# Kernel tuning notes

Measured on AMD Instinct MI355X. Metric: run time of the kernel, lower is better.

## Reference

```python
import jax, jax.numpy as jnp
import numpy as np

BETA = 0.5
ITEM_NUM = 100000
REGION_NUM = 1000
EMBED = 128
HIDDEN = 256
B, H = 1024, 256


def setup_inputs() -> dict:
    key = jax.random.key(0)
    ks = jax.random.split(key, 10)
    history = jax.random.randint(ks[0], (B, H), 0, ITEM_NUM)
    target = jax.random.randint(ks[1], (B,), 0, ITEM_NUM)
    history_region = jax.random.randint(ks[2], (B, H), 0, REGION_NUM)
    target_region = jax.random.randint(ks[3], (B,), 0, REGION_NUM)
    E_hist = 0.01 * jax.random.normal(ks[4], (ITEM_NUM, EMBED), dtype=jnp.float32)
    E_targ = 0.01 * jax.random.normal(ks[5], (ITEM_NUM, EMBED), dtype=jnp.float32)
    E_reg = 0.01 * jax.random.normal(ks[6], (REGION_NUM, EMBED), dtype=jnp.float32)
    lim1 = 1.0 / np.sqrt(2 * EMBED)
    W1 = jax.random.uniform(ks[7], (2 * EMBED, HIDDEN), jnp.float32, -lim1, lim1)
    b1 = jnp.zeros((HIDDEN,), jnp.float32)
    lim2 = 1.0 / np.sqrt(HIDDEN)
    w2 = jax.random.uniform(ks[8], (HIDDEN,), jnp.float32, -lim2, lim2)
    return {"history": history, "target": target,
            "history_region": history_region, "target_region": target_region,
            "E_hist": E_hist, "E_targ": E_targ, "E_reg": E_reg,
            "W1": W1, "b1": b1, "w2": w2}


def reference(history, target, history_region, target_region,
              E_hist, E_targ, E_reg, W1, b1, w2):
    # gathers + concat: hist [B,H,2d], tgt [B,2d]
    hist = jnp.concatenate([E_hist[history], E_reg[history_region]], axis=-1)
    tgt = jnp.concatenate([E_targ[target], E_reg[target_region]], axis=-1)
    # elementwise product broadcast over history dim
    inp = hist * tgt[:, None, :]                      # [B,H,2d]
    hid = jax.nn.relu(jnp.einsum('bhd,dk->bhk', inp, W1) + b1)
    scores = jnp.einsum('bhk,k->bh', hid, w2)         # [B,H]
    mask = (history != target[:, None]).astype(scores.dtype)
    exp_a = jnp.exp(scores) * mask                    # [B,H]
    denom = jnp.power(jnp.sum(exp_a, axis=-1), BETA)  # [B]
    attn = exp_a / denom[:, None]                     # [B,H]
    # weighted reduction: sum_h sum_d hist*attn*tgt
    pred = jnp.einsum('bhd,bh,bd->b', hist, attn, tgt)
    return jax.nn.sigmoid(pred)
```

## Files before the change

### kernel.cpp

```cpp
#include <hip/hip_runtime.h>
#include <hip/hip_bf16.h>

#define NB 1024
#define NH 256
#define EMB 128
#define TWOD 256
#define HID 256
#define ROWS 128
#define NBLK (NB * 2)

typedef __attribute__((ext_vector_type(4))) float f32x4;
typedef __attribute__((ext_vector_type(8))) short bf16x8;

__device__ __forceinline__ unsigned short f2bf(float f) {
  union { float f; unsigned u; } v; v.f = f;
  unsigned u = v.u;
  unsigned r = (u + 0x7fffu + ((u >> 16) & 1u)) >> 16;
  return (unsigned short)r;
}

__global__ __launch_bounds__(256) void prep_w1t(const float* __restrict__ W1,
                                                unsigned short* __restrict__ W1T) {
  const int d = blockIdx.x;
  const int n = threadIdx.x;
  W1T[(size_t)n * TWOD + d] = f2bf(W1[(size_t)d * HID + n]);
}

__global__ __launch_bounds__(256) void prep_tgt(const int* __restrict__ target,
                                                const int* __restrict__ tregion,
                                                const float* __restrict__ E_targ,
                                                const float* __restrict__ E_reg,
                                                float* __restrict__ tgtv) {
  const int b = blockIdx.x;
  const int c = threadIdx.x;
  float v = (c < EMB) ? E_targ[(size_t)target[b] * EMB + c]
                      : E_reg[(size_t)tregion[b] * EMB + (c - EMB)];
  tgtv[(size_t)b * TWOD + c] = v;
}

__global__ __launch_bounds__(256) void zero_acc(float* __restrict__ p) {
  p[blockIdx.x * 256 + threadIdx.x] = 0.f;
}

__global__ __launch_bounds__(512, 4) void nais_main(
    const int* __restrict__ history, const int* __restrict__ target,
    const int* __restrict__ hregion,
    const float* __restrict__ E_hist, const float* __restrict__ E_reg,
    const unsigned short* __restrict__ W1T, const float* __restrict__ b1,
    const float* __restrict__ w2, const float* __restrict__ tgtv,
    float* __restrict__ acc_se, float* __restrict__ acc_sd)
{
  const int blk = blockIdx.x;
  const int b = blk >> 1;
  const int r0 = (blk & 1) * ROWS;
  const int tid = threadIdx.x;
  const int lane = tid & 63;
  const int wave = tid >> 6;
  const int l15 = lane & 15;
  const int lhi = lane >> 4;
  const int l31 = lane & 31;
  const int halfsel = lane >> 5;

  __shared__ __align__(16) unsigned short inp_lds[ROWS * 256];
  __shared__ float dot_lds[ROWS];
  __shared__ float score_parts[8][ROWS];

  const int tgt_item = target[b];

  {
    const f32x4 t = *(const f32x4*)(tgtv + (size_t)b * TWOD + halfsel * EMB + l31 * 4);
    const int* keysrc = halfsel ? hregion : history;
    const float* table = halfsel ? E_reg : E_hist;

    int key[16];
    #pragma unroll
    for (int s = 0; s < 16; ++s)
      key[s] = keysrc[b * NH + r0 + wave * 16 + s];

    f32x4 vb[16];
    #pragma unroll
    for (int s = 0; s < 16; ++s)
      vb[s] = *(const f32x4*)(table + (size_t)key[s] * EMB + l31 * 4);

    #pragma unroll
    for (int s = 0; s < 16; ++s) {
      const int row = wave * 16 + s;
      f32x4 v = vb[s] * t;
      float ds = v[0] + v[1] + v[2] + v[3];
      ds += __shfl_xor(ds, 1);
      ds += __shfl_xor(ds, 2);
      ds += __shfl_xor(ds, 4);
      ds += __shfl_xor(ds, 8);
      ds += __shfl_xor(ds, 16);
      ds += __shfl_xor(ds, 32);
      if (lane == 0) dot_lds[row] = ds;

      float2 f01; f01.x = v[0]; f01.y = v[1];
      float2 f23; f23.x = v[2]; f23.y = v[3];
      __hip_bfloat162 p0 = __float22bfloat162_rn(f01);
      __hip_bfloat162 p1 = __float22bfloat162_rn(f23);
      union { __hip_bfloat162 h; unsigned u; } c0, c1;
      c0.h = p0; c1.h = p1;
      const int g = halfsel * 16 + (l31 >> 1);
      const int gs = g ^ (row & 7) ^ ((g >> 3) & 3);
      unsigned* dst = (unsigned*)&inp_lds[row * 256 + gs * 8 + (lane & 1) * 4];
      dst[0] = c0.u; dst[1] = c1.u;
    }
  }
  __syncthreads();

  bf16x8 bfr[8][2];
  float b1v[2], w2v[2];
  #pragma unroll
  for (int n = 0; n < 2; ++n) {
    const int colh = wave * 32 + n * 16 + l15;
    b1v[n] = b1[colh];
    w2v[n] = w2[colh];
    #pragma unroll
    for (int kk = 0; kk < 8; ++kk)
      bfr[kk][n] = *(const bf16x8*)(W1T + (size_t)colh * TWOD + kk * 32 + lhi * 8);
  }

  #pragma unroll
  for (int c = 0; c < 2; ++c) {
    f32x4 acc[4][2];
    #pragma unroll
    for (int m = 0; m < 4; ++m)
      #pragma unroll
      for (int n = 0; n < 2; ++n)
        acc[m][n] = (f32x4){0.f, 0.f, 0.f, 0.f};

    #pragma unroll
    for (int kk = 0; kk < 8; ++kk) {
      bf16x8 af[4];
      #pragma unroll
      for (int m = 0; m < 4; ++m) {
        const int row = c * 64 + m * 16 + l15;
        const int gk = kk * 4 + lhi;
        const int gs = gk ^ (row & 7) ^ ((gk >> 3) & 3);
        af[m] = *(const bf16x8*)(&inp_lds[row * 256 + gs * 8]);
      }
      #pragma unroll
      for (int m = 0; m < 4; ++m)
        #pragma unroll
        for (int n = 0; n < 2; ++n)
          acc[m][n] = __builtin_amdgcn_mfma_f32_16x16x32_bf16(af[m], bfr[kk][n], acc[m][n], 0, 0, 0);
    }

    #pragma unroll
    for (int m = 0; m < 4; ++m) {
      #pragma unroll
      for (int r = 0; r < 4; ++r) {
        float p = 0.f;
        #pragma unroll
        for (int n = 0; n < 2; ++n) {
          float hv = acc[m][n][r] + b1v[n];
          hv = hv > 0.f ? hv : 0.f;
          p += hv * w2v[n];
        }
        p += __shfl_xor(p, 1);
        p += __shfl_xor(p, 2);
        p += __shfl_xor(p, 4);
        p += __shfl_xor(p, 8);
        if (l15 == 0) score_parts[wave][c * 64 + m * 16 + lhi * 4 + r] = p;
      }
    }
  }
  __syncthreads();

  if (wave < 2) {
    const int lrow = wave * 64 + lane;
    float sc = 0.f;
    #pragma unroll
    for (int w = 0; w < 8; ++w) sc += score_parts[w][lrow];
    const int item = history[b * NH + r0 + lrow];
    float e = (item != tgt_item) ? expf(sc) : 0.f;
    float ed = e * dot_lds[lrow];
    #pragma unroll
    for (int off = 32; off >= 1; off >>= 1) {
      e += __shfl_xor(e, off);
      ed += __shfl_xor(ed, off);
    }
    if (lane == 0) {
      atomicAdd(&acc_se[b], e);
      atomicAdd(&acc_sd[b], ed);
    }
  }
}

__global__ __launch_bounds__(256) void finalize(const float* __restrict__ acc_se,
                                                const float* __restrict__ acc_sd,
                                                float* __restrict__ out) {
  const int b = blockIdx.x * 256 + threadIdx.x;
  if (b < NB) {
    const float se = acc_se[b];
    const float sd = acc_sd[b];
    const float pred = (se > 0.f) ? (sd / sqrtf(se)) : 0.f;
    out[b] = 1.f / (1.f + expf(-pred));
  }
}

extern "C" void kernel_launch(void* const* d_in, const int* in_sizes, int n_in,
                              void* d_out, int out_size, void* d_ws, size_t ws_size,
                              hipStream_t stream) {
  const int* history = (const int*)d_in[0];
  const int* target  = (const int*)d_in[1];
  const int* hregion = (const int*)d_in[2];
  const int* tregion = (const int*)d_in[3];
  const float* E_hist = (const float*)d_in[4];
  const float* E_targ = (const float*)d_in[5];
  const float* E_reg  = (const float*)d_in[6];
  const float* W1 = (const float*)d_in[7];
  const float* b1 = (const float*)d_in[8];
  const float* w2 = (const float*)d_in[9];
  float* out = (float*)d_out;

  unsigned short* W1T = (unsigned short*)d_ws;
  char* p = (char*)d_ws + (size_t)TWOD * HID * sizeof(unsigned short);
  float* tgtv = (float*)p;           p += (size_t)NB * TWOD * sizeof(float);
  float* acc_se = (float*)p;         p += (size_t)NB * sizeof(float);
  float* acc_sd = (float*)p;

  zero_acc<<<(2 * NB) / 256, 256, 0, stream>>>(acc_se);
  prep_w1t<<<TWOD, HID, 0, stream>>>(W1, W1T);
  prep_tgt<<<NB, TWOD, 0, stream>>>(target, tregion, E_targ, E_reg, tgtv);
  nais_main<<<NBLK, 512, 0, stream>>>(history, target, hregion, E_hist, E_reg,
                                      W1T, b1, w2, tgtv, acc_se, acc_sd);
  finalize<<<(NB + 255) / 256, 256, 0, stream>>>(acc_se, acc_sd, out);
}
```

Before: 96.34 us.

## Split each batch row across four 256-thread blocks and drop atomics

Each block now handles 64 history rows with 4 waves instead of 128 rows with 8 waves, giving 4096 smaller blocks and halving LDS per block. Each wave now covers 64 hidden columns in two passes, reloading a W1 slice per pass. Per-block partial sums are written to a buffer and summed in finalize, which removes the zeroing kernel and the atomics. MFMA loops are also wrapped in s_setprio. The risk is doubled W1 fragment loads per block and more block-launch overhead.

```diff
diff --git a/kernel.cpp b/kernel.cpp
--- a/kernel.cpp
+++ b/kernel.cpp
@@ -6,8 +6,9 @@
 #define EMB 128
 #define TWOD 256
 #define HID 256
-#define ROWS 128
-#define NBLK (NB * 2)
+#define ROWS 64
+#define BPB 4
+#define NBLK (NB * BPB)
 
 typedef __attribute__((ext_vector_type(4))) float f32x4;
 typedef __attribute__((ext_vector_type(8))) short bf16x8;
@@ -38,21 +39,17 @@
   tgtv[(size_t)b * TWOD + c] = v;
 }
 
-__global__ __launch_bounds__(256) void zero_acc(float* __restrict__ p) {
-  p[blockIdx.x * 256 + threadIdx.x] = 0.f;
-}
-
-__global__ __launch_bounds__(512, 4) void nais_main(
+__global__ __launch_bounds__(256, 4) void nais_main(
     const int* __restrict__ history, const int* __restrict__ target,
     const int* __restrict__ hregion,
     const float* __restrict__ E_hist, const float* __restrict__ E_reg,
     const unsigned short* __restrict__ W1T, const float* __restrict__ b1,
     const float* __restrict__ w2, const float* __restrict__ tgtv,
-    float* __restrict__ acc_se, float* __restrict__ acc_sd)
+    float* __restrict__ part_se, float* __restrict__ part_sd)
 {
   const int blk = blockIdx.x;
-  const int b = blk >> 1;
-  const int r0 = (blk & 1) * ROWS;
+  const int b = blk >> 2;
+  const int r0 = (blk & 3) * ROWS;
   const int tid = threadIdx.x;
   const int lane = tid & 63;
   const int wave = tid >> 6;
@@ -109,20 +106,22 @@
   }
   __syncthreads();
 
-  bf16x8 bfr[8][2];
-  float b1v[2], w2v[2];
   #pragma unroll
-  for (int n = 0; n < 2; ++n) {
-    const int colh = wave * 32 + n * 16 + l15;
-    b1v[n] = b1[colh];
-    w2v[n] = w2[colh];
-    #pragma unroll
-    for (int kk = 0; kk < 8; ++kk)
-      bfr[kk][n] = *(const bf16x8*)(W1T + (size_t)colh * TWOD + kk * 32 + lhi * 8);
-  }
-
-  #pragma unroll
-  for (int c = 0; c < 2; ++c) {
+  for (int cp = 0; cp < 2; ++cp) {
+    const int col0 = wave * 64 + cp * 32;
+
+    bf16x8 bfr[8][2];
+    float b1v[2], w2v[2];
+    #pragma unroll
+    for (int n = 0; n < 2; ++n) {
+      const int colh = col0 + n * 16 + l15;
+      b1v[n] = b1[colh];
+      w2v[n] = w2[colh];
+      #pragma unroll
+      for (int kk = 0; kk < 8; ++kk)
+        bfr[kk][n] = *(const bf16x8*)(W1T + (size_t)colh * TWOD + kk * 32 + lhi * 8);
+    }
+
     f32x4 acc[4][2];
     #pragma unroll
     for (int m = 0; m < 4; ++m)
@@ -130,12 +129,13 @@
       for (int n = 0; n < 2; ++n)
         acc[m][n] = (f32x4){0.f, 0.f, 0.f, 0.f};
 
+    __builtin_amdgcn_s_setprio(1);
     #pragma unroll
     for (int kk = 0; kk < 8; ++kk) {
       bf16x8 af[4];
       #pragma unroll
       for (int m = 0; m < 4; ++m) {
-        const int row = c * 64 + m * 16 + l15;
+        const int row = m * 16 + l15;
         const int gk = kk * 4 + lhi;
         const int gs = gk ^ (row & 7) ^ ((gk >> 3) & 3);
         af[m] = *(const bf16x8*)(&inp_lds[row * 256 + gs * 8]);
@@ -146,7 +146,9 @@
         for (int n = 0; n < 2; ++n)
           acc[m][n] = __builtin_amdgcn_mfma_f32_16x16x32_bf16(af[m], bfr[kk][n], acc[m][n], 0, 0, 0);
     }
-
+    __builtin_amdgcn_s_setprio(0);
+
+    const int strip = wave * 2 + cp;
     #pragma unroll
     for (int m = 0; m < 4; ++m) {
       #pragma unroll
@@ -162,39 +164,42 @@
         p += __shfl_xor(p, 2);
         p += __shfl_xor(p, 4);
         p += __shfl_xor(p, 8);
-        if (l15 == 0) score_parts[wave][c * 64 + m * 16 + lhi * 4 + r] = p;
+        if (l15 == 0) score_parts[strip][m * 16 + lhi * 4 + r] = p;
       }
     }
   }
   __syncthreads();
 
-  if (wave < 2) {
-    const int lrow = wave * 64 + lane;
+  if (wave == 0) {
     float sc = 0.f;
     #pragma unroll
-    for (int w = 0; w < 8; ++w) sc += score_parts[w][lrow];
-    const int item = history[b * NH + r0 + lrow];
+    for (int w = 0; w < 8; ++w) sc += score_parts[w][lane];
+    const int item = history[b * NH + r0 + lane];
     float e = (item != tgt_item) ? expf(sc) : 0.f;
-    float ed = e * dot_lds[lrow];
+    float ed = e * dot_lds[lane];
     #pragma unroll
     for (int off = 32; off >= 1; off >>= 1) {
       e += __shfl_xor(e, off);
       ed += __shfl_xor(ed, off);
     }
     if (lane == 0) {
-      atomicAdd(&acc_se[b], e);
-      atomicAdd(&acc_sd[b], ed);
-    }
-  }
-}
-
-__global__ __launch_bounds__(256) void finalize(const float* __restrict__ acc_se,
-                                                const float* __restrict__ acc_sd,
+      part_se[blk] = e;
+      part_sd[blk] = ed;
+    }
+  }
+}
+
+__global__ __launch_bounds__(256) void finalize(const float* __restrict__ part_se,
+                                                const float* __restrict__ part_sd,
                                                 float* __restrict__ out) {
   const int b = blockIdx.x * 256 + threadIdx.x;
   if (b < NB) {
-    const float se = acc_se[b];
-    const float sd = acc_sd[b];
+    float se = 0.f, sd = 0.f;
+    #pragma unroll
+    for (int i = 0; i < BPB; ++i) {
+      se += part_se[b * BPB + i];
+      sd += part_sd[b * BPB + i];
+    }
     const float pred = (se > 0.f) ? (sd / sqrtf(se)) : 0.f;
     out[b] = 1.f / (1.f + expf(-pred));
   }
@@ -218,13 +223,12 @@
   unsigned short* W1T = (unsigned short*)d_ws;
   char* p = (char*)d_ws + (size_t)TWOD * HID * sizeof(unsigned short);
   float* tgtv = (float*)p;           p += (size_t)NB * TWOD * sizeof(float);
-  float* acc_se = (float*)p;         p += (size_t)NB * sizeof(float);
-  float* acc_sd = (float*)p;
-
-  zero_acc<<<(2 * NB) / 256, 256, 0, stream>>>(acc_se);
+  float* part_se = (float*)p;        p += (size_t)NBLK * sizeof(float);
+  float* part_sd = (float*)p;
+
   prep_w1t<<<TWOD, HID, 0, stream>>>(W1, W1T);
   prep_tgt<<<NB, TWOD, 0, stream>>>(target, tregion, E_targ, E_reg, tgtv);
-  nais_main<<<NBLK, 512, 0, stream>>>(history, target, hregion, E_hist, E_reg,
-                                      W1T, b1, w2, tgtv, acc_se, acc_sd);
-  finalize<<<(NB + 255) / 256, 256, 0, stream>>>(acc_se, acc_sd, out);
-}
+  nais_main<<<NBLK, 256, 0, stream>>>(history, target, hregion, E_hist, E_reg,
+                                      W1T, b1, w2, tgtv, part_se, part_sd);
+  finalize<<<(NB + 255) / 256, 256, 0, stream>>>(part_se, part_sd, out);
+}
```

New measurement: 102.4 us. 6.3% more time.

## Fuse target gather into main kernel and replace atomics with partial sums

Applied to the files above, without the earlier changes.

Removes the prep_tgt and zero_acc launches by gathering the target embedding directly in the main kernel. Per-block results go to a partial-sum buffer instead of atomicAdd, and finalize reduces those partials. History keys are cached in LDS so they are not reloaded from global memory. The MFMA loop now loads W1T fragments per k-step instead of holding them all in registers, and wraps the MFMAs in s_setprio. The aims are fewer launches and lower register pressure, at the cost of more global loads of W1T.

```diff
diff --git a/kernel.cpp b/kernel.cpp
--- a/kernel.cpp
+++ b/kernel.cpp
@@ -7,7 +7,8 @@
 #define TWOD 256
 #define HID 256
 #define ROWS 128
-#define NBLK (NB * 2)
+#define BPB 2
+#define NBLK (NB * BPB)
 
 typedef __attribute__((ext_vector_type(4))) float f32x4;
 typedef __attribute__((ext_vector_type(8))) short bf16x8;
@@ -26,29 +27,14 @@
   W1T[(size_t)n * TWOD + d] = f2bf(W1[(size_t)d * HID + n]);
 }
 
-__global__ __launch_bounds__(256) void prep_tgt(const int* __restrict__ target,
-                                                const int* __restrict__ tregion,
-                                                const float* __restrict__ E_targ,
-                                                const float* __restrict__ E_reg,
-                                                float* __restrict__ tgtv) {
-  const int b = blockIdx.x;
-  const int c = threadIdx.x;
-  float v = (c < EMB) ? E_targ[(size_t)target[b] * EMB + c]
-                      : E_reg[(size_t)tregion[b] * EMB + (c - EMB)];
-  tgtv[(size_t)b * TWOD + c] = v;
-}
-
-__global__ __launch_bounds__(256) void zero_acc(float* __restrict__ p) {
-  p[blockIdx.x * 256 + threadIdx.x] = 0.f;
-}
-
 __global__ __launch_bounds__(512, 4) void nais_main(
     const int* __restrict__ history, const int* __restrict__ target,
-    const int* __restrict__ hregion,
-    const float* __restrict__ E_hist, const float* __restrict__ E_reg,
+    const int* __restrict__ hregion, const int* __restrict__ tregion,
+    const float* __restrict__ E_hist, const float* __restrict__ E_targ,
+    const float* __restrict__ E_reg,
     const unsigned short* __restrict__ W1T, const float* __restrict__ b1,
-    const float* __restrict__ w2, const float* __restrict__ tgtv,
-    float* __restrict__ acc_se, float* __restrict__ acc_sd)
+    const float* __restrict__ w2,
+    float* __restrict__ part_se, float* __restrict__ part_sd)
 {
   const int blk = blockIdx.x;
   const int b = blk >> 1;
@@ -63,15 +49,18 @@
 
   __shared__ __align__(16) unsigned short inp_lds[ROWS * 256];
   __shared__ float dot_lds[ROWS];
+  __shared__ int items_lds[ROWS];
   __shared__ float score_parts[8][ROWS];
 
+  const float* tsrc = halfsel ? (E_reg + (size_t)tregion[b] * EMB)
+                              : (E_targ + (size_t)target[b] * EMB);
+  const f32x4 t = *(const f32x4*)(tsrc + l31 * 4);
   const int tgt_item = target[b];
 
+  const int* keysrc = halfsel ? hregion : history;
+  const float* table = halfsel ? E_reg : E_hist;
+
   {
-    const f32x4 t = *(const f32x4*)(tgtv + (size_t)b * TWOD + halfsel * EMB + l31 * 4);
-    const int* keysrc = halfsel ? hregion : history;
-    const float* table = halfsel ? E_reg : E_hist;
-
     int key[16];
     #pragma unroll
     for (int s = 0; s < 16; ++s)
@@ -85,6 +74,7 @@
     #pragma unroll
     for (int s = 0; s < 16; ++s) {
       const int row = wave * 16 + s;
+      if (lane == 0) items_lds[row] = key[s];
       f32x4 v = vb[s] * t;
       float ds = v[0] + v[1] + v[2] + v[3];
       ds += __shfl_xor(ds, 1);
@@ -109,60 +99,73 @@
   }
   __syncthreads();
 
-  bf16x8 bfr[8][2];
-  float b1v[2], w2v[2];
-  #pragma unroll
-  for (int n = 0; n < 2; ++n) {
-    const int colh = wave * 32 + n * 16 + l15;
-    b1v[n] = b1[colh];
-    w2v[n] = w2[colh];
-    #pragma unroll
-    for (int kk = 0; kk < 8; ++kk)
-      bfr[kk][n] = *(const bf16x8*)(W1T + (size_t)colh * TWOD + kk * 32 + lhi * 8);
-  }
-
-  #pragma unroll
-  for (int c = 0; c < 2; ++c) {
-    f32x4 acc[4][2];
-    #pragma unroll
-    for (int m = 0; m < 4; ++m)
-      #pragma unroll
-      for (int n = 0; n < 2; ++n)
-        acc[m][n] = (f32x4){0.f, 0.f, 0.f, 0.f};
+  {
+    const int col0 = wave * 32;
+    float b1v[2], w2v[2];
+    #pragma unroll
+    for (int n = 0; n < 2; ++n) {
+      const int colh = col0 + n * 16 + l15;
+      b1v[n] = b1[colh];
+      w2v[n] = w2[colh];
+    }
+
+    f32x4 acc[2][4][2];
+    #pragma unroll
+    for (int c = 0; c < 2; ++c)
+      #pragma unroll
+      for (int m = 0; m < 4; ++m)
+        #pragma unroll
+        for (int n = 0; n < 2; ++n)
+          acc[c][m][n] = (f32x4){0.f, 0.f, 0.f, 0.f};
 
     #pragma unroll
     for (int kk = 0; kk < 8; ++kk) {
-      bf16x8 af[4];
+      bf16x8 bfr[2];
+      #pragma unroll
+      for (int n = 0; n < 2; ++n) {
+        const int colh = col0 + n * 16 + l15;
+        bfr[n] = *(const bf16x8*)(W1T + (size_t)colh * TWOD + kk * 32 + lhi * 8);
+      }
+      bf16x8 af[2][4];
+      #pragma unroll
+      for (int c = 0; c < 2; ++c)
+        #pragma unroll
+        for (int m = 0; m < 4; ++m) {
+          const int row = c * 64 + m * 16 + l15;
+          const int gk = kk * 4 + lhi;
+          const int gs = gk ^ (row & 7) ^ ((gk >> 3) & 3);
+          af[c][m] = *(const bf16x8*)(&inp_lds[row * 256 + gs * 8]);
+        }
+      __builtin_amdgcn_s_setprio(1);
+      #pragma unroll
+      for (int c = 0; c < 2; ++c)
+        #pragma unroll
+        for (int m = 0; m < 4; ++m)
+          #pragma unroll
+          for (int n = 0; n < 2; ++n)
+            acc[c][m][n] = __builtin_amdgcn_mfma_f32_16x16x32_bf16(af[c][m], bfr[n], acc[c][m][n], 0, 0, 0);
+      __builtin_amdgcn_s_setprio(0);
+    }
+
+    #pragma unroll
+    for (int c = 0; c < 2; ++c) {
       #pragma unroll
       for (int m = 0; m < 4; ++m) {
-        const int row = c * 64 + m * 16 + l15;
-        const int gk = kk * 4 + lhi;
-        const int gs = gk ^ (row & 7) ^ ((gk >> 3) & 3);
-        af[m] = *(const bf16x8*)(&inp_lds[row * 256 + gs * 8]);
-      }
-      #pragma unroll
-      for (int m = 0; m < 4; ++m)
-        #pragma unroll
-        for (int n = 0; n < 2; ++n)
-          acc[m][n] = __builtin_amdgcn_mfma_f32_16x16x32_bf16(af[m], bfr[kk][n], acc[m][n], 0, 0, 0);
-    }
-
-    #pragma unroll
-    for (int m = 0; m < 4; ++m) {
-      #pragma unroll
-      for (int r = 0; r < 4; ++r) {
-        float p = 0.f;
-        #pragma unroll
-        for (int n = 0; n < 2; ++n) {
-          float hv = acc[m][n][r] + b1v[n];
-          hv = hv > 0.f ? hv : 0.f;
-          p += hv * w2v[n];
+        #pragma unroll
+        for (int r = 0; r < 4; ++r) {
+          float p = 0.f;
+          #pragma unroll
+          for (int n = 0; n < 2; ++n) {
+            float hv = acc[c][m][n][r] + b1v[n];
+            hv = hv > 0.f ? hv : 0.f;
+            p += hv * w2v[n];
+          }
+          p += __shfl_xor(p, 1);
+          p += __shfl_xor(p, 2);
+          p += __shfl_xor(p, 4);
+          p += __shfl_xor(p, 8);
+          if (l15 == 0) score_parts[wave][c * 64 + m * 16 + lhi * 4 + r] = p;
         }
-        p += __shfl_xor(p, 1);
-        p += __shfl_xor(p, 2);
-        p += __shfl_xor(p, 4);
-        p += __shfl_xor(p, 8);
-        if (l15 == 0) score_parts[wave][c * 64 + m * 16 + lhi * 4 + r] = p;
       }
     }
   }
@@ -173,8 +176,7 @@
     float sc = 0.f;
     #pragma unroll
     for (int w = 0; w < 8; ++w) sc += score_parts[w][lrow];
-    const int item = history[b * NH + r0 + lrow];
-    float e = (item != tgt_item) ? expf(sc) : 0.f;
+    float e = (items_lds[lrow] != tgt_item) ? expf(sc) : 0.f;
     float ed = e * dot_lds[lrow];
     #pragma unroll
     for (int off = 32; off >= 1; off >>= 1) {
@@ -182,19 +184,23 @@
       ed += __shfl_xor(ed, off);
     }
     if (lane == 0) {
-      atomicAdd(&acc_se[b], e);
-      atomicAdd(&acc_sd[b], ed);
-    }
-  }
-}
-
-__global__ __launch_bounds__(256) void finalize(const float* __restrict__ acc_se,
-                                                const float* __restrict__ acc_sd,
+      part_se[blk * 2 + wave] = e;
+      part_sd[blk * 2 + wave] = ed;
+    }
+  }
+}
+
+__global__ __launch_bounds__(256) void finalize(const float* __restrict__ part_se,
+                                                const float* __restrict__ part_sd,
                                                 float* __restrict__ out) {
   const int b = blockIdx.x * 256 + threadIdx.x;
   if (b < NB) {
-    const float se = acc_se[b];
-    const float sd = acc_sd[b];
+    float se = 0.f, sd = 0.f;
+    #pragma unroll
+    for (int i = 0; i < BPB * 2; ++i) {
+      se += part_se[b * BPB * 2 + i];
+      sd += part_sd[b * BPB * 2 + i];
+    }
     const float pred = (se > 0.f) ? (sd / sqrtf(se)) : 0.f;
     out[b] = 1.f / (1.f + expf(-pred));
   }
@@ -217,14 +223,12 @@
 
   unsigned short* W1T = (unsigned short*)d_ws;
   char* p = (char*)d_ws + (size_t)TWOD * HID * sizeof(unsigned short);
-  float* tgtv = (float*)p;           p += (size_t)NB * TWOD * sizeof(float);
-  float* acc_se = (float*)p;         p += (size_t)NB * sizeof(float);
-  float* acc_sd = (float*)p;
-
-  zero_acc<<<(2 * NB) / 256, 256, 0, stream>>>(acc_se);
+  float* part_se = (float*)p;        p += (size_t)NBLK * 2 * sizeof(float);
+  float* part_sd = (float*)p;
+
   prep_w1t<<<TWOD, HID, 0, stream>>>(W1, W1T);
-  prep_tgt<<<NB, TWOD, 0, stream>>>(target, tregion, E_targ, E_reg, tgtv);
-  nais_main<<<NBLK, 512, 0, stream>>>(history, target, hregion, E_hist, E_reg,
-                                      W1T, b1, w2, tgtv, acc_se, acc_sd);
-  finalize<<<(NB + 255) / 256, 256, 0, stream>>>(acc_se, acc_sd, out);
-}
+  nais_main<<<NBLK, 512, 0, stream>>>(history, target, hregion, tregion,
+                                      E_hist, E_targ, E_reg, W1T, b1, w2,
+                                      part_se, part_sd);
+  finalize<<<(NB + 255) / 256, 256, 0, stream>>>(part_se, part_sd, out);
+}
```

Result: faster. 89.49 us (-7.1%).
